# Optimization experiments

Measured on AMD Instinct MI355X. Metric: run time of the kernel, lower is better.

## Reference

```python
import jax, jax.numpy as jnp
import numpy as np

N_BINS = 15
TEMP = 1.0


def setup_inputs() -> dict:
    key = jax.random.key(0)
    k1, k2 = jax.random.split(key)
    N, C = 1000000, 100
    probs = jax.random.uniform(k1, (N, C), dtype=jnp.float32)
    labels = jax.random.randint(k2, (N,), 0, C, dtype=jnp.int64)
    return {"probs": probs, "labels": labels}


def reference(probs, labels):
    # apply_log=True, temp=1.0: p = softmax(log(probs)/temp)
    p = jax.nn.softmax(jnp.log(probs) / TEMP, axis=-1)  # [N, C]
    confidences = jnp.max(p, axis=1)                     # [N]
    predictions = jnp.argmax(p, axis=1)                  # [N]
    accuracies = (predictions == labels).astype(p.dtype)

    one_hot = jax.nn.one_hot(labels, p.shape[-1], dtype=p.dtype)
    bri = jnp.mean(jnp.sum((p - one_hot) ** 2, axis=1))  # mean squared L2 norm

    # bins are (i/n_bins, (i+1)/n_bins]; conf > 0 always (softmax max >= 1/C)
    bin_idx = jnp.clip(jnp.ceil(confidences * N_BINS).astype(jnp.int32) - 1, 0, N_BINS - 1)

    ones = jnp.ones_like(confidences)
    counts = jax.ops.segment_sum(ones, bin_idx, num_segments=N_BINS)
    sum_conf = jax.ops.segment_sum(confidences, bin_idx, num_segments=N_BINS)
    sum_acc = jax.ops.segment_sum(accuracies, bin_idx, num_segments=N_BINS)

    nonempty = counts > 0
    safe = jnp.maximum(counts, 1.0)
    gap = jnp.where(nonempty, jnp.abs(sum_conf / safe - sum_acc / safe), 0.0)  # [n_bins]
    prop = counts / confidences.shape[0]

    ece = jnp.sum(gap * prop)
    max_err = jnp.max(gap)  # matches torch init of 0.0 for all-empty case
    return jnp.stack([ece, max_err, bri])
```

## Files before the change

kernel.cpp:

```cpp
#include <hip/hip_runtime.h>

#define NBINS 15

__global__ __launch_bounds__(256) void ece_rows(const float* __restrict__ probs,
                                                const int* __restrict__ labels,
                                                int N, int C,
                                                double* __restrict__ g_bri,
                                                float* __restrict__ g_cnt,
                                                float* __restrict__ g_conf,
                                                float* __restrict__ g_acc) {
    __shared__ float s_cnt[NBINS], s_conf[NBINS], s_acc[NBINS];
    __shared__ float s_bri;
    const int tid = threadIdx.x;
    if (tid < NBINS) { s_cnt[tid] = 0.f; s_conf[tid] = 0.f; s_acc[tid] = 0.f; }
    if (tid == 0) s_bri = 0.f;
    __syncthreads();

    float tbri = 0.f;
    const int stride = gridDim.x * blockDim.x;

    for (int r = blockIdx.x * blockDim.x + tid; r < N; r += stride) {
        const float* row = probs + (size_t)r * (size_t)C;
        const int label = labels[r];
        float sum = 0.f, sq = 0.f, vmax = -1.f, pl;
        int imax = 0;

        if (C == 100) {
            pl = row[label];
            const float4* row4 = (const float4*)row;
            float4 v[25];
            #pragma unroll
            for (int k = 0; k < 25; k++) v[k] = row4[k];

            #pragma unroll
            for (int k = 0; k < 25; k++) {
                float4 u = v[k];
                sum += (u.x + u.y) + (u.z + u.w);
                sq = fmaf(u.x, u.x, sq);
                sq = fmaf(u.y, u.y, sq);
                sq = fmaf(u.z, u.z, sq);
                sq = fmaf(u.w, u.w, sq);
                int c = k * 4;
                if (u.x > vmax) { vmax = u.x; imax = c; }
                if (u.y > vmax) { vmax = u.y; imax = c + 1; }
                if (u.z > vmax) { vmax = u.z; imax = c + 2; }
                if (u.w > vmax) { vmax = u.w; imax = c + 3; }
            }
        } else {
            pl = row[label];
            for (int c = 0; c < C; c++) {
                float v = row[c];
                sum += v;
                sq = fmaf(v, v, sq);
                if (v > vmax) { vmax = v; imax = c; }
            }
        }

        const float inv = 1.f / sum;
        const float conf = vmax * inv;
        const float acc = (imax == label) ? 1.f : 0.f;
        const float bri = sq * inv * inv - 2.f * (pl * inv) + 1.f;

        int bin = (int)ceilf(conf * (float)NBINS) - 1;
        bin = bin < 0 ? 0 : (bin > NBINS - 1 ? NBINS - 1 : bin);

        atomicAdd(&s_cnt[bin], 1.f);
        atomicAdd(&s_conf[bin], conf);
        atomicAdd(&s_acc[bin], acc);
        tbri += bri;
    }

    #pragma unroll
    for (int off = 32; off > 0; off >>= 1)
        tbri += __shfl_down(tbri, off);
    if ((tid & 63) == 0) atomicAdd(&s_bri, tbri);
    __syncthreads();

    if (tid < NBINS) {
        atomicAdd(&g_cnt[tid], s_cnt[tid]);
        atomicAdd(&g_conf[tid], s_conf[tid]);
        atomicAdd(&g_acc[tid], s_acc[tid]);
    }
    if (tid == 0) atomicAdd(g_bri, (double)s_bri);
}

__global__ void ece_final(const double* __restrict__ g_bri,
                          const float* __restrict__ g_cnt,
                          const float* __restrict__ g_conf,
                          const float* __restrict__ g_acc,
                          float* __restrict__ out, float invN) {
    if (threadIdx.x == 0 && blockIdx.x == 0) {
        float ece = 0.f, mx = 0.f;
        for (int b = 0; b < NBINS; b++) {
            float c = g_cnt[b];
            float gap = 0.f;
            if (c > 0.f) gap = fabsf(g_conf[b] / c - g_acc[b] / c);
            ece += gap * (c * invN);
            if (gap > mx) mx = gap;
        }
        out[0] = ece;
        out[1] = mx;
        out[2] = (float)(g_bri[0] * (double)invN);
    }
}

extern "C" void kernel_launch(void* const* d_in, const int* in_sizes, int n_in,
                              void* d_out, int out_size, void* d_ws, size_t ws_size,
                              hipStream_t stream) {
    const float* probs  = (const float*)d_in[0];
    const int*   labels = (const int*)d_in[1];
    const int N = in_sizes[1];
    const int C = in_sizes[0] / N;

    double* g_bri  = (double*)d_ws;
    float*  g_cnt  = (float*)((char*)d_ws + sizeof(double));
    float*  g_conf = g_cnt + NBINS;
    float*  g_acc  = g_conf + NBINS;

    hipMemsetAsync(d_ws, 0, sizeof(double) + 3 * NBINS * sizeof(float), stream);

    const int blocks = 1024;
    hipLaunchKernelGGL(ece_rows, dim3(blocks), dim3(256), 0, stream,
                       probs, labels, N, C, g_bri, g_cnt, g_conf, g_acc);
    hipLaunchKernelGGL(ece_final, dim3(1), dim3(64), 0, stream,
                       g_bri, g_cnt, g_conf, g_acc, (float*)d_out, 1.f / (float)N);
}
```

Before: 611.4 us.

## Split each row across four lanes for coalesced loads and per-group histograms

Each row is now handled by a group of four lanes that load interleaved float4 chunks, so adjacent lanes read adjacent memory instead of each thread streaming its own 400-byte row. Partial sum, sum-of-squares and argmax are combined with xor shuffles (ties go to the lower index), and one lane per row updates a private per-group shared histogram without atomics; the groups are reduced at block end. The grid is doubled to 2048 blocks. The general-C fallback is dropped and C is hardcoded to 100.

```diff
diff --git a/kernel.cpp b/kernel.cpp
--- a/kernel.cpp
+++ b/kernel.cpp
@@ -9,65 +9,80 @@
                                                 float* __restrict__ g_cnt,
                                                 float* __restrict__ g_conf,
                                                 float* __restrict__ g_acc) {
-    __shared__ float s_cnt[NBINS], s_conf[NBINS], s_acc[NBINS];
+    __shared__ float s_hist[3][64][NBINS];
     __shared__ float s_bri;
     const int tid = threadIdx.x;
-    if (tid < NBINS) { s_cnt[tid] = 0.f; s_conf[tid] = 0.f; s_acc[tid] = 0.f; }
+    for (int i = tid; i < 3 * 64 * NBINS; i += 256)
+        ((float*)s_hist)[i] = 0.f;
     if (tid == 0) s_bri = 0.f;
     __syncthreads();
 
+    const int l   = tid & 3;
+    const int grp = tid >> 2;
     float tbri = 0.f;
-    const int stride = gridDim.x * blockDim.x;
 
-    for (int r = blockIdx.x * blockDim.x + tid; r < N; r += stride) {
-        const float* row = probs + (size_t)r * (size_t)C;
-        const int label = labels[r];
-        float sum = 0.f, sq = 0.f, vmax = -1.f, pl;
+    const int r0      = blockIdx.x * 64 + grp;
+    const int rstride = gridDim.x * 64;
+
+    for (int r = r0; r < N; r += rstride) {
+        const float4* row4 = (const float4*)(probs + (size_t)r * 100);
+
+        float4 v[6];
+        #pragma unroll
+        for (int j = 0; j < 6; j++) v[j] = row4[j * 4 + l];
+
+        float sum = 0.f, sq = 0.f, vmax = -1.f;
         int imax = 0;
-
-        if (C == 100) {
-            pl = row[label];
-            const float4* row4 = (const float4*)row;
-            float4 v[25];
-            #pragma unroll
-            for (int k = 0; k < 25; k++) v[k] = row4[k];
-
-            #pragma unroll
-            for (int k = 0; k < 25; k++) {
-                float4 u = v[k];
-                sum += (u.x + u.y) + (u.z + u.w);
-                sq = fmaf(u.x, u.x, sq);
-                sq = fmaf(u.y, u.y, sq);
-                sq = fmaf(u.z, u.z, sq);
-                sq = fmaf(u.w, u.w, sq);
-                int c = k * 4;
-                if (u.x > vmax) { vmax = u.x; imax = c; }
-                if (u.y > vmax) { vmax = u.y; imax = c + 1; }
-                if (u.z > vmax) { vmax = u.z; imax = c + 2; }
-                if (u.w > vmax) { vmax = u.w; imax = c + 3; }
-            }
-        } else {
-            pl = row[label];
-            for (int c = 0; c < C; c++) {
-                float v = row[c];
-                sum += v;
-                sq = fmaf(v, v, sq);
-                if (v > vmax) { vmax = v; imax = c; }
-            }
+        #pragma unroll
+        for (int j = 0; j < 6; j++) {
+            float4 u = v[j];
+            int c = (j * 4 + l) * 4;
+            sum += (u.x + u.y) + (u.z + u.w);
+            sq = fmaf(u.x, u.x, sq);
+            sq = fmaf(u.y, u.y, sq);
+            sq = fmaf(u.z, u.z, sq);
+            sq = fmaf(u.w, u.w, sq);
+            if (u.x > vmax) { vmax = u.x; imax = c; }
+            if (u.y > vmax) { vmax = u.y; imax = c + 1; }
+            if (u.z > vmax) { vmax = u.z; imax = c + 2; }
+            if (u.w > vmax) { vmax = u.w; imax = c + 3; }
+        }
+        if (l == 0) {
+            float4 u = row4[24];
+            sum += (u.x + u.y) + (u.z + u.w);
+            sq = fmaf(u.x, u.x, sq);
+            sq = fmaf(u.y, u.y, sq);
+            sq = fmaf(u.z, u.z, sq);
+            sq = fmaf(u.w, u.w, sq);
+            if (u.x > vmax) { vmax = u.x; imax = 96; }
+            if (u.y > vmax) { vmax = u.y; imax = 97; }
+            if (u.z > vmax) { vmax = u.z; imax = 98; }
+            if (u.w > vmax) { vmax = u.w; imax = 99; }
         }
 
-        const float inv = 1.f / sum;
-        const float conf = vmax * inv;
-        const float acc = (imax == label) ? 1.f : 0.f;
-        const float bri = sq * inv * inv - 2.f * (pl * inv) + 1.f;
+        #pragma unroll
+        for (int off = 1; off <= 2; off <<= 1) {
+            sum += __shfl_xor(sum, off);
+            sq  += __shfl_xor(sq,  off);
+            float ov = __shfl_xor(vmax, off);
+            int   oi = __shfl_xor(imax, off);
+            if (ov > vmax || (ov == vmax && oi < imax)) { vmax = ov; imax = oi; }
+        }
 
-        int bin = (int)ceilf(conf * (float)NBINS) - 1;
-        bin = bin < 0 ? 0 : (bin > NBINS - 1 ? NBINS - 1 : bin);
+        if (l == 0) {
+            const int label = labels[r];
+            const float pl = ((const float*)row4)[label];
+            const float inv = 1.f / sum;
+            const float conf = vmax * inv;
+            const float acc = (imax == label) ? 1.f : 0.f;
+            tbri += sq * inv * inv - 2.f * (pl * inv) + 1.f;
 
-        atomicAdd(&s_cnt[bin], 1.f);
-        atomicAdd(&s_conf[bin], conf);
-        atomicAdd(&s_acc[bin], acc);
-        tbri += bri;
+            int bin = (int)ceilf(conf * (float)NBINS) - 1;
+            bin = bin < 0 ? 0 : (bin > NBINS - 1 ? NBINS - 1 : bin);
+            s_hist[0][grp][bin] += 1.f;
+            s_hist[1][grp][bin] += conf;
+            s_hist[2][grp][bin] += acc;
+        }
     }
 
     #pragma unroll
@@ -76,10 +91,13 @@
     if ((tid & 63) == 0) atomicAdd(&s_bri, tbri);
     __syncthreads();
 
-    if (tid < NBINS) {
-        atomicAdd(&g_cnt[tid], s_cnt[tid]);
-        atomicAdd(&g_conf[tid], s_conf[tid]);
-        atomicAdd(&g_acc[tid], s_acc[tid]);
+    if (tid < 3 * NBINS) {
+        const int a = tid / NBINS, b = tid % NBINS;
+        float acc = 0.f;
+        #pragma unroll
+        for (int g = 0; g < 64; g++) acc += s_hist[a][g][b];
+        float* dst = (a == 0) ? g_cnt : (a == 1) ? g_conf : g_acc;
+        atomicAdd(&dst[b], acc);
     }
     if (tid == 0) atomicAdd(g_bri, (double)s_bri);
 }
@@ -110,7 +128,6 @@
     const float* probs  = (const float*)d_in[0];
     const int*   labels = (const int*)d_in[1];
     const int N = in_sizes[1];
-    const int C = in_sizes[0] / N;
 
     double* g_bri  = (double*)d_ws;
     float*  g_cnt  = (float*)((char*)d_ws + sizeof(double));
@@ -119,9 +136,9 @@
 
     hipMemsetAsync(d_ws, 0, sizeof(double) + 3 * NBINS * sizeof(float), stream);
 
-    const int blocks = 1024;
+    const int blocks = 2048;
     hipLaunchKernelGGL(ece_rows, dim3(blocks), dim3(256), 0, stream,
-                       probs, labels, N, C, g_bri, g_cnt, g_conf, g_acc);
+                       probs, labels, N, 100, g_bri, g_cnt, g_conf, g_acc);
     hipLaunchKernelGGL(ece_final, dim3(1), dim3(64), 0, stream,
                        g_bri, g_cnt, g_conf, g_acc, (float*)d_out, 1.f / (float)N);
 }
```

Result: faster. 546.1 us (-10.7%).
